# Performance work log

Hardware: AMD Instinct MI355X
Metric: run time of the kernel (lower is better)

## Reference

```python
import jax, jax.numpy as jnp
import numpy as np

EMBED_DIM = 1024
B, S = 4, 2048

def setup_inputs() -> dict:
    key = jax.random.key(0)
    ks = jax.random.split(key, 9)
    D = EMBED_DIM
    scale = 1.0 / np.sqrt(D)
    scale2 = 1.0 / np.sqrt(2 * D)
    return {
        "classical_state": jax.random.normal(ks[0], (B, S, D), jnp.float32),
        "quantum_state": jax.random.normal(ks[1], (B, S, D), jnp.float32),
        "Wc": jax.random.uniform(ks[2], (D, D), jnp.float32, -scale, scale),
        "bc": jax.random.uniform(ks[3], (D,), jnp.float32, -scale, scale),
        "Wq": jax.random.uniform(ks[4], (D, D), jnp.float32, -scale, scale),
        "bq": jax.random.uniform(ks[5], (D,), jnp.float32, -scale, scale),
        "Wg": jax.random.uniform(ks[6], (D, 2 * D), jnp.float32, -scale2, scale2),
        "bg": jax.random.uniform(ks[7], (D,), jnp.float32, -scale2, scale2),
        "temperature": jnp.array(1.0, jnp.float32),
    }

def reference(classical_state, quantum_state, Wc, bc, Wq, bq, Wg, bg, temperature):
    D = classical_state.shape[-1]
    c_proj = jnp.einsum('bsd,ed->bse', classical_state, Wc) + bc  # [B,S,D]
    q_proj = jnp.einsum('bsd,ed->bse', quantum_state, Wq) + bq    # [B,S,D]
    combined = jnp.concatenate([c_proj, q_proj], axis=-1)         # [B,S,2D]
    interface_state = jax.nn.sigmoid(jnp.einsum('bsf,ef->bse', combined, Wg) + bg)
    similarity = jnp.einsum('bsd,btd->bst', c_proj, q_proj) / jnp.sqrt(jnp.asarray(D, c_proj.dtype))
    attention_weights = jax.nn.softmax(similarity / temperature, axis=-1)  # [B,S,S]
    transfer_state = jnp.einsum('bst,btd->bsd', attention_weights, quantum_state)
    return classical_state + interface_state * transfer_state
```

## Files before the change

### kernel.cpp

```cpp
#include <hip/hip_runtime.h>


typedef unsigned short u16;
typedef unsigned char u8;
typedef __bf16 bf16x8 __attribute__((ext_vector_type(8)));
typedef float f32x4 __attribute__((ext_vector_type(4)));

__device__ __forceinline__ u16 f2bf(float f) {
    unsigned int x;
    __builtin_memcpy(&x, &f, 4);
    unsigned int r = x + 0x7FFFu + ((x >> 16) & 1u);
    return (u16)(r >> 16);
}
__device__ __forceinline__ float bf2f(u16 u) {
    unsigned int x = ((unsigned int)u) << 16;
    float f;
    __builtin_memcpy(&f, &x, 4);
    return f;
}
__device__ __forceinline__ u8 f2fp8(float f) {
    int p = __builtin_amdgcn_cvt_pk_fp8_f32(f, f, 0, false);
    return (u8)(p & 0xFF);
}

__device__ __forceinline__ void xcd_tile(int& tx, int& ty) {
    const int gx = gridDim.x;
    const int nwg = gx * gridDim.y;
    const int l = blockIdx.x + gx * blockIdx.y;
    const int per = nwg >> 3;
    const int swz = (l & 7) * per + (l >> 3);
    tx = swz % gx;
    ty = swz / gx;
}

#define GLOBAL_TO_LDS16(gp, lp)                                                           \
    __builtin_amdgcn_global_load_lds((const __attribute__((address_space(1))) void*)(gp), \
                                     (__attribute__((address_space(3))) void*)(lp), 16, 0, 0)

__global__ __launch_bounds__(256, 2) void gemm_proj(
    const u16* __restrict__ A0, long sAz, int lda,
    const u16* __restrict__ Bp, long sBz, int ldb,
    u8* __restrict__ C8, long sCz, int ldc, int K,
    const float* __restrict__ bias, long sBiasZ) {
    __shared__ __align__(16) u16 As[128 * 64];
    __shared__ __align__(16) u16 Bs[128 * 64];

    const int tid  = threadIdx.x;
    const int lane = tid & 63;
    const int wave = tid >> 6;
    const int z    = blockIdx.z;

    const u16* a = A0 + (long)z * sAz;
    const u16* b = Bp + (long)z * sBz;

    int tx, ty;
    xcd_tile(tx, ty);
    const int tileM = ty * 128;
    const int tileN = tx * 128;

    const int wm  = wave >> 1;
    const int wn  = wave & 1;
    const int r16 = lane & 15;
    const int kg  = lane >> 4;

    const int srow = lane >> 3;
    const int sgc  = ((lane & 7) ^ (lane >> 3)) * 8;
    const int swb  = r16 & 7;

    f32x4 acc[4][4] = {};

    for (int k0 = 0; k0 < K; k0 += 64) {
#pragma unroll
        for (int p = 0; p < 4; p++) {
            const int rbase = p * 32 + wave * 8;
            GLOBAL_TO_LDS16(a + (long)(tileM + rbase + srow) * lda + k0 + sgc, &As[rbase * 64]);
            GLOBAL_TO_LDS16(b + (long)(tileN + rbase + srow) * ldb + k0 + sgc, &Bs[rbase * 64]);
        }
        __syncthreads();

        bf16x8 af[2][4], bfr[2][4];
#pragma unroll
        for (int h = 0; h < 2; h++) {
#pragma unroll
            for (int i = 0; i < 4; i++) {
                const int Ra = wm * 64 + i * 16 + r16;
                af[h][i]  = *(const bf16x8*)&As[Ra * 64 + (((h * 4 + kg) ^ swb)) * 8];
                const int Rb = wn * 64 + i * 16 + r16;
                bfr[h][i] = *(const bf16x8*)&Bs[Rb * 64 + (((h * 4 + kg) ^ swb)) * 8];
            }
        }
#pragma unroll
        for (int h = 0; h < 2; h++)
#pragma unroll
            for (int i = 0; i < 4; i++)
#pragma unroll
                for (int j = 0; j < 4; j++)
                    acc[i][j] = __builtin_amdgcn_mfma_f32_16x16x32_bf16(
                        af[h][i], bfr[h][j], acc[i][j], 0, 0, 0);
        __syncthreads();
    }

#pragma unroll
    for (int i = 0; i < 4; i++)
#pragma unroll
        for (int j = 0; j < 4; j++) {
            int col = tileN + wn * 64 + j * 16 + r16;
            float bv = bias[(long)z * sBiasZ + col];
#pragma unroll
            for (int v = 0; v < 4; v++) {
                int row = tileM + wm * 64 + i * 16 + kg * 4 + v;
                C8[(long)z * sCz + (long)row * ldc + col] = f2fp8(acc[i][j][v] + bv);
            }
        }
}

template <int MODE>
__global__ __launch_bounds__(256, 2) void gemm8(
    const u8* __restrict__ A0, const u8* __restrict__ A1, long sAz, int lda, int kSplit,
    const u8* __restrict__ Bp, long sBz, int ldb,
    void* __restrict__ Cp, long cOff, long sCz, int ldc, int K,
    const float* __restrict__ bias, const float* __restrict__ temp,
    const float* __restrict__ cls, const u16* __restrict__ g16,
    float* __restrict__ lsum, long lSz) {
    __shared__ __align__(16) u8 As[128 * 128];
    __shared__ __align__(16) u8 Bs[128 * 128];

    const int tid  = threadIdx.x;
    const int lane = tid & 63;
    const int wave = tid >> 6;
    const int z    = blockIdx.z;

    const u8* a = A0 + (long)z * sAz;
    const u8* b = Bp + (long)z * sBz;

    int tx, ty;
    xcd_tile(tx, ty);
    const int tileM = ty * 128;
    const int tileN = tx * 128;

    const int wm  = wave >> 1;
    const int wn  = wave & 1;
    const int r16 = lane & 15;
    const int kg  = lane >> 4;

    const int srow = lane >> 3;
    const int sgc  = ((lane & 7) ^ (lane >> 3)) * 16;

    f32x4 acc[4][4] = {};

    for (int k0 = 0; k0 < K; k0 += 128) {
        const u8* Ap = a;
        int kA = k0;
        if (MODE == 1 && k0 >= kSplit) { Ap = A1; kA = k0 - kSplit; }

#pragma unroll
        for (int p = 0; p < 4; p++) {
            const int rbase = p * 32 + wave * 8;
            GLOBAL_TO_LDS16(Ap + (long)(tileM + rbase + srow) * lda + kA + sgc, &As[rbase * 128]);
            GLOBAL_TO_LDS16(b + (long)(tileN + rbase + srow) * ldb + k0 + sgc, &Bs[rbase * 128]);
        }
        __syncthreads();

#pragma unroll
        for (int h = 0; h < 4; h++) {
            long af[4], bfr[4];
#pragma unroll
            for (int i = 0; i < 4; i++) {
                const int Ra = wm * 64 + i * 16 + r16;
                af[i]  = *(const long*)&As[Ra * 128 + (((h * 2 + (kg >> 1)) ^ (Ra & 7))) * 16 + (kg & 1) * 8];
                const int Rb = wn * 64 + i * 16 + r16;
                bfr[i] = *(const long*)&Bs[Rb * 128 + (((h * 2 + (kg >> 1)) ^ (Rb & 7))) * 16 + (kg & 1) * 8];
            }
#pragma unroll
            for (int i = 0; i < 4; i++)
#pragma unroll
                for (int j = 0; j < 4; j++)
                    acc[i][j] = __builtin_amdgcn_mfma_f32_16x16x32_fp8_fp8(
                        af[i], bfr[j], acc[i][j], 0, 0, 0);
        }
        __syncthreads();
    }

    float scale = 1.0f;
    if (MODE == 2) scale = 1.0f / (32.0f * temp[0]);

    u16*   C16 = (u16*)Cp;
    u8*    C8  = (u8*)Cp;
    float* C32 = (float*)Cp;

#pragma unroll
    for (int i = 0; i < 4; i++) {
        float rs[4] = {0.f, 0.f, 0.f, 0.f};
#pragma unroll
        for (int j = 0; j < 4; j++) {
            int col = tileN + wn * 64 + j * 16 + r16;
            float bv = (MODE == 1) ? bias[col] : 0.0f;
#pragma unroll
            for (int v = 0; v < 4; v++) {
                int row = tileM + wm * 64 + i * 16 + kg * 4 + v;
                long idx = cOff + (long)z * sCz + (long)row * ldc + col;
                float val = acc[i][j][v];
                if (MODE == 1) {
                    C16[idx] = f2bf(1.0f / (1.0f + __expf(-(val + bv))));
                } else if (MODE == 2) {
                    float e = __expf(val * scale);
                    C8[idx] = f2fp8(e);
                    rs[v] += e;
                } else {
                    float inv = 1.0f / lsum[(long)z * lSz + row];
                    C32[idx] = cls[idx] + bf2f(g16[idx]) * (val * inv);
                }
            }
        }
        if (MODE == 2) {
#pragma unroll
            for (int v = 0; v < 4; v++) {
                float s = rs[v];
#pragma unroll
                for (int off = 1; off < 16; off <<= 1) s += __shfl_xor(s, off, 64);
                if (r16 == 0) {
                    int row = tileM + wm * 64 + i * 16 + kg * 4 + v;
                    atomicAdd(&lsum[(long)z * lSz + row], s);
                }
            }
        }
    }
}

__global__ __launch_bounds__(256) void convert_bf16(const f32x4* __restrict__ s,
                                                    ushort4* __restrict__ d, long n4) {
    long i = (long)blockIdx.x * 256 + threadIdx.x;
    long stride = (long)gridDim.x * 256;
    for (; i < n4; i += stride) {
        f32x4 v = s[i];
        ushort4 o;
        o.x = f2bf(v.x); o.y = f2bf(v.y); o.z = f2bf(v.z); o.w = f2bf(v.w);
        d[i] = o;
    }
}

__global__ __launch_bounds__(256) void convert_fp8(const f32x4* __restrict__ s,
                                                   unsigned int* __restrict__ d, long n4) {
    long i = (long)blockIdx.x * 256 + threadIdx.x;
    long stride = (long)gridDim.x * 256;
    for (; i < n4; i += stride) {
        f32x4 v = s[i];
        int w = __builtin_amdgcn_cvt_pk_fp8_f32(v.x, v.y, 0, false);
        w = __builtin_amdgcn_cvt_pk_fp8_f32(v.z, v.w, w, true);
        d[i] = (unsigned int)w;
    }
}

__global__ __launch_bounds__(256) void zero_f32(float* __restrict__ p, int n) {
    int i = blockIdx.x * 256 + threadIdx.x;
    if (i < n) p[i] = 0.0f;
}

__global__ __launch_bounds__(256) void transpose_fp8(const u16* __restrict__ Q,
                                                     u8* __restrict__ QT, int S, int D) {
    __shared__ u8 tile[64][65];
    int bz = blockIdx.z;
    const u16* q = Q + (long)bz * S * D;
    u8* qt = QT + (long)bz * S * D;
    int t0 = blockIdx.x * 64;
    int d0 = blockIdx.y * 64;
    int c = threadIdx.x & 63;
    int r = threadIdx.x >> 6;
#pragma unroll
    for (int i = 0; i < 16; i++) {
        int tl = r + 4 * i;
        tile[tl][c] = f2fp8(bf2f(q[(long)(t0 + tl) * D + d0 + c]));
    }
    __syncthreads();
#pragma unroll
    for (int i = 0; i < 16; i++) {
        int dl = r + 4 * i;
        qt[(long)(d0 + dl) * S + t0 + c] = tile[c][dl];
    }
}

extern "C" void kernel_launch(void* const* d_in, const int* in_sizes, int n_in,
                              void* d_out, int out_size, void* d_ws, size_t ws_size,
                              hipStream_t stream) {
    (void)in_sizes; (void)n_in; (void)out_size;

    const float* classical = (const float*)d_in[0];
    const float* quantum   = (const float*)d_in[1];
    const float* Wc        = (const float*)d_in[2];
    const float* bc        = (const float*)d_in[3];
    const float* Wq        = (const float*)d_in[4];
    const float* bq        = (const float*)d_in[5];
    const float* Wg        = (const float*)d_in[6];
    const float* bg        = (const float*)d_in[7];
    const float* temp      = (const float*)d_in[8];
    float* out = (float*)d_out;

    const int B = 4, S = 2048, D = 1024;
    const long MD = (long)B * S * D;

    float* l       = (float*)d_ws;
    float* biasCat = l + (long)B * S;
    u16* cls_b = (u16*)(biasCat + 2 * D);
    u16* qnt_b = cls_b + MD;
    u16* Wc_b  = qnt_b + MD;
    u16* Wq_b  = Wc_b + (long)D * D;
    u8*  Wg8   = (u8*)(Wq_b + (long)D * D);
    u8*  cp8   = Wg8 + (long)D * 2 * D;
    u8*  qp8   = cp8 + MD;
    u8*  qT8   = qp8 + MD;
    u8*  P8    = qT8 + MD;
    u16* g     = cls_b;

    const size_t fixed_bytes = (size_t)B * S * 4 + 2 * D * 4 +
        (size_t)(2 * MD + 2 * (long)D * D) * 2 + (size_t)D * 2 * D + 3 * (size_t)MD;
    int CH = 128;
    for (int c = 2048; c >= 128; c >>= 1) {
        if (ws_size >= fixed_bytes + (size_t)B * c * S) { CH = c; break; }
    }

    dim3 blk(256);

    convert_bf16<<<1024, blk, 0, stream>>>((const f32x4*)classical, (ushort4*)cls_b, MD / 4);
    convert_bf16<<<1024, blk, 0, stream>>>((const f32x4*)quantum, (ushort4*)qnt_b, MD / 4);
    convert_bf16<<<256, blk, 0, stream>>>((const f32x4*)Wc, (ushort4*)Wc_b, (long)D * D / 4);
    convert_bf16<<<256, blk, 0, stream>>>((const f32x4*)Wq, (ushort4*)Wq_b, (long)D * D / 4);
    convert_fp8<<<512, blk, 0, stream>>>((const f32x4*)Wg, (unsigned int*)Wg8, (long)D * 2 * D / 4);
    hipMemcpyAsync(biasCat, bc, D * sizeof(float), hipMemcpyDeviceToDevice, stream);
    hipMemcpyAsync(biasCat + D, bq, D * sizeof(float), hipMemcpyDeviceToDevice, stream);
    zero_f32<<<dim3((B * S + 255) / 256), blk, 0, stream>>>(l, B * S);

    gemm_proj<<<dim3(D / 128, (B * S) / 128, 2), blk, 0, stream>>>(
        cls_b, MD, D, Wc_b, (long)D * D, D, cp8, MD, D, D, biasCat, D);

    gemm8<1><<<dim3(D / 128, (B * S) / 128, 1), blk, 0, stream>>>(
        cp8, qp8, 0, D, D, Wg8, 0, 2 * D, g, 0, 0, D, 2 * D,
        bg, nullptr, nullptr, nullptr, nullptr, 0);

    transpose_fp8<<<dim3(S / 64, D / 64, B), blk, 0, stream>>>(qnt_b, qT8, S, D);

    for (int m0 = 0; m0 < S; m0 += CH) {
        gemm8<2><<<dim3(S / 128, CH / 128, B), blk, 0, stream>>>(
            cp8 + (long)m0 * D, nullptr, (long)S * D, D, 1 << 30,
            qp8, (long)S * D, D, P8, 0, (long)CH * S, S, D,
            nullptr, temp, nullptr, nullptr, l + m0, S);
        gemm8<4><<<dim3(D / 128, CH / 128, B), blk, 0, stream>>>(
            P8, nullptr, (long)CH * S, S, 1 << 30, qT8, (long)D * S, S,
            out, (long)m0 * D, (long)S * D, D, S,
            nullptr, nullptr, classical, g, l + m0, S);
    }
}
```

Baseline: 296.5 us.

## Double-buffer FP8 GEMMs with larger 256-row tiles and 512-thread blocks

Replaces the single-buffered 128x128 FP8 GEMM with a templated kernel that uses 256-row tiles (256 or 128 columns), 8 waves per block, and double-buffered LDS. The next K-tile's global-to-LDS loads are interleaved with MFMA phases, and setprio raises wave priority around the MFMA bursts. The intent is to hide global load latency and raise data reuse per tile. In exchange it uses much more LDS per block (up to 128KB), which can limit occupancy. The chunk size minimum also rises to 256 rows.

```diff
diff --git a/kernel.cpp b/kernel.cpp
--- a/kernel.cpp
+++ b/kernel.cpp
@@ -114,16 +114,23 @@
         }
 }
 
-template <int MODE>
-__global__ __launch_bounds__(256, 2) void gemm8(
+template <int MODE, int BN, int WM, int WN>
+__global__ __launch_bounds__(512, 2) void gemm8b(
     const u8* __restrict__ A0, const u8* __restrict__ A1, long sAz, int lda, int kSplit,
     const u8* __restrict__ Bp, long sBz, int ldb,
     void* __restrict__ Cp, long cOff, long sCz, int ldc, int K,
     const float* __restrict__ bias, const float* __restrict__ temp,
     const float* __restrict__ cls, const u16* __restrict__ g16,
     float* __restrict__ lsum, long lSz) {
-    __shared__ __align__(16) u8 As[128 * 128];
-    __shared__ __align__(16) u8 Bs[128 * 128];
+    constexpr int BM  = 256;
+    constexpr int BK  = 128;
+    constexpr int MR  = BM / WM / 16;
+    constexpr int NR  = BN / WN / 16;
+    constexpr int NPH = (MR / 2) * (NR / 2);
+    constexpr int BSTG = BN / 64;
+
+    __shared__ __align__(16) u8 As[2][BM * BK];
+    __shared__ __align__(16) u8 Bs[2][BN * BK];
 
     const int tid  = threadIdx.x;
     const int lane = tid & 63;
@@ -135,50 +142,97 @@
 
     int tx, ty;
     xcd_tile(tx, ty);
-    const int tileM = ty * 128;
-    const int tileN = tx * 128;
-
-    const int wm  = wave >> 1;
-    const int wn  = wave & 1;
+    const int tileM = ty * BM;
+    const int tileN = tx * BN;
+
+    const int wm  = wave / WN;
+    const int wn  = wave % WN;
     const int r16 = lane & 15;
     const int kg  = lane >> 4;
 
     const int srow = lane >> 3;
     const int sgc  = ((lane & 7) ^ (lane >> 3)) * 16;
 
-    f32x4 acc[4][4] = {};
-
-    for (int k0 = 0; k0 < K; k0 += 128) {
+    auto stageA = [&](int buf, int t, int p) {
         const u8* Ap = a;
-        int kA = k0;
-        if (MODE == 1 && k0 >= kSplit) { Ap = A1; kA = k0 - kSplit; }
-
-#pragma unroll
-        for (int p = 0; p < 4; p++) {
-            const int rbase = p * 32 + wave * 8;
-            GLOBAL_TO_LDS16(Ap + (long)(tileM + rbase + srow) * lda + kA + sgc, &As[rbase * 128]);
-            GLOBAL_TO_LDS16(b + (long)(tileN + rbase + srow) * ldb + k0 + sgc, &Bs[rbase * 128]);
-        }
-        __syncthreads();
-
-#pragma unroll
-        for (int h = 0; h < 4; h++) {
-            long af[4], bfr[4];
-#pragma unroll
-            for (int i = 0; i < 4; i++) {
-                const int Ra = wm * 64 + i * 16 + r16;
-                af[i]  = *(const long*)&As[Ra * 128 + (((h * 2 + (kg >> 1)) ^ (Ra & 7))) * 16 + (kg & 1) * 8];
-                const int Rb = wn * 64 + i * 16 + r16;
-                bfr[i] = *(const long*)&Bs[Rb * 128 + (((h * 2 + (kg >> 1)) ^ (Rb & 7))) * 16 + (kg & 1) * 8];
-            }
-#pragma unroll
-            for (int i = 0; i < 4; i++)
-#pragma unroll
-                for (int j = 0; j < 4; j++)
-                    acc[i][j] = __builtin_amdgcn_mfma_f32_16x16x32_fp8_fp8(
-                        af[i], bfr[j], acc[i][j], 0, 0, 0);
-        }
-        __syncthreads();
+        int kA = t * BK;
+        if (MODE == 1 && kA >= kSplit) { Ap = A1; kA -= kSplit; }
+        const int rbase = p * 64 + wave * 8;
+        GLOBAL_TO_LDS16(Ap + (long)(tileM + rbase + srow) * lda + kA + sgc,
+                        &As[buf][rbase * BK]);
+    };
+    auto stageB = [&](int buf, int t, int p) {
+        const int rbase = p * 64 + wave * 8;
+        GLOBAL_TO_LDS16(b + (long)(tileN + rbase + srow) * ldb + t * BK + sgc,
+                        &Bs[buf][rbase * BK]);
+    };
+
+    f32x4 acc[MR][NR] = {};
+
+    const int nt = K / BK;
+#pragma unroll
+    for (int p = 0; p < 4; p++) stageA(0, 0, p);
+#pragma unroll
+    for (int p = 0; p < BSTG; p++) stageB(0, 0, p);
+
+    for (int t = 0; t < nt; t++) {
+        const int cur = t & 1, nxt = cur ^ 1;
+        const bool pf = (t + 1 < nt);
+        asm volatile("s_waitcnt vmcnt(0)" ::: "memory");
+        __builtin_amdgcn_s_barrier();
+        asm volatile("" ::: "memory");
+
+#pragma unroll
+        for (int ph = 0; ph < NPH; ph++) {
+            const int i0 = (ph / (NR / 2)) * 2;
+            const int j0 = (ph % (NR / 2)) * 2;
+
+            long af[2][4], bfv[2][4];
+#pragma unroll
+            for (int ii = 0; ii < 2; ii++) {
+                const int Ra = wm * (BM / WM) + (i0 + ii) * 16 + r16;
+#pragma unroll
+                for (int ks = 0; ks < 4; ks++) {
+                    const int c = 2 * ks + (kg >> 1);
+                    af[ii][ks] = *(const long*)&As[cur][Ra * BK + ((c ^ (Ra & 7)) << 4) + (kg & 1) * 8];
+                }
+            }
+#pragma unroll
+            for (int jj = 0; jj < 2; jj++) {
+                const int Rb = wn * (BN / WN) + (j0 + jj) * 16 + r16;
+#pragma unroll
+                for (int ks = 0; ks < 4; ks++) {
+                    const int c = 2 * ks + (kg >> 1);
+                    bfv[jj][ks] = *(const long*)&Bs[cur][Rb * BK + ((c ^ (Rb & 7)) << 4) + (kg & 1) * 8];
+                }
+            }
+
+            if (pf) {
+                if (BN == 128) {
+                    if (ph == 0) { stageA(nxt, t + 1, 0); stageA(nxt, t + 1, 1); }
+                    if (ph == 1) { stageA(nxt, t + 1, 2); stageA(nxt, t + 1, 3); }
+                    if (ph == 2) { stageB(nxt, t + 1, 0); }
+                    if (ph == 3) { stageB(nxt, t + 1, 1); }
+                } else {
+                    if ((ph & 1) == 0) stageA(nxt, t + 1, ph >> 1);
+                    else               stageB(nxt, t + 1, ph >> 1);
+                }
+            }
+
+            __builtin_amdgcn_s_barrier();
+            __builtin_amdgcn_s_setprio(1);
+#pragma unroll
+            for (int ks = 0; ks < 4; ks++)
+#pragma unroll
+                for (int ii = 0; ii < 2; ii++)
+#pragma unroll
+                    for (int jj = 0; jj < 2; jj++)
+                        acc[i0 + ii][j0 + jj] = __builtin_amdgcn_mfma_f32_16x16x32_fp8_fp8(
+                            af[ii][ks], bfv[jj][ks], acc[i0 + ii][j0 + jj], 0, 0, 0);
+            __builtin_amdgcn_s_setprio(0);
+            __builtin_amdgcn_s_barrier();
+            asm volatile("" ::: "memory");
+        }
     }
 
     float scale = 1.0f;
@@ -189,15 +243,15 @@
     float* C32 = (float*)Cp;
 
 #pragma unroll
-    for (int i = 0; i < 4; i++) {
+    for (int i = 0; i < MR; i++) {
         float rs[4] = {0.f, 0.f, 0.f, 0.f};
 #pragma unroll
-        for (int j = 0; j < 4; j++) {
-            int col = tileN + wn * 64 + j * 16 + r16;
+        for (int j = 0; j < NR; j++) {
+            int col = tileN + wn * (BN / WN) + j * 16 + r16;
             float bv = (MODE == 1) ? bias[col] : 0.0f;
 #pragma unroll
             for (int v = 0; v < 4; v++) {
-                int row = tileM + wm * 64 + i * 16 + kg * 4 + v;
+                int row = tileM + wm * (BM / WM) + i * 16 + kg * 4 + v;
                 long idx = cOff + (long)z * sCz + (long)row * ldc + col;
                 float val = acc[i][j][v];
                 if (MODE == 1) {
@@ -219,7 +273,7 @@
 #pragma unroll
                 for (int off = 1; off < 16; off <<= 1) s += __shfl_xor(s, off, 64);
                 if (r16 == 0) {
-                    int row = tileM + wm * 64 + i * 16 + kg * 4 + v;
+                    int row = tileM + wm * (BM / WM) + i * 16 + kg * 4 + v;
                     atomicAdd(&lsum[(long)z * lSz + row], s);
                 }
             }
@@ -313,12 +367,13 @@
 
     const size_t fixed_bytes = (size_t)B * S * 4 + 2 * D * 4 +
         (size_t)(2 * MD + 2 * (long)D * D) * 2 + (size_t)D * 2 * D + 3 * (size_t)MD;
-    int CH = 128;
-    for (int c = 2048; c >= 128; c >>= 1) {
+    int CH = 256;
+    for (int c = 2048; c >= 256; c >>= 1) {
         if (ws_size >= fixed_bytes + (size_t)B * c * S) { CH = c; break; }
     }
 
     dim3 blk(256);
+    dim3 blk8(512);
 
     convert_bf16<<<1024, blk, 0, stream>>>((const f32x4*)classical, (ushort4*)cls_b, MD / 4);
     convert_bf16<<<1024, blk, 0, stream>>>((const f32x4*)quantum, (ushort4*)qnt_b, MD / 4);
@@ -332,18 +387,18 @@
     gemm_proj<<<dim3(D / 128, (B * S) / 128, 2), blk, 0, stream>>>(
         cls_b, MD, D, Wc_b, (long)D * D, D, cp8, MD, D, D, biasCat, D);
 
-    gemm8<1><<<dim3(D / 128, (B * S) / 128, 1), blk, 0, stream>>>(
+    gemm8b<1, 128, 4, 2><<<dim3(D / 128, (B * S) / 256, 1), blk8, 0, stream>>>(
         cp8, qp8, 0, D, D, Wg8, 0, 2 * D, g, 0, 0, D, 2 * D,
         bg, nullptr, nullptr, nullptr, nullptr, 0);
 
     transpose_fp8<<<dim3(S / 64, D / 64, B), blk, 0, stream>>>(qnt_b, qT8, S, D);
 
     for (int m0 = 0; m0 < S; m0 += CH) {
-        gemm8<2><<<dim3(S / 128, CH / 128, B), blk, 0, stream>>>(
+        gemm8b<2, 256, 2, 4><<<dim3(S / 256, CH / 256, B), blk8, 0, stream>>>(
             cp8 + (long)m0 * D, nullptr, (long)S * D, D, 1 << 30,
             qp8, (long)S * D, D, P8, 0, (long)CH * S, S, D,
             nullptr, temp, nullptr, nullptr, l + m0, S);
-        gemm8<4><<<dim3(D / 128, CH / 128, B), blk, 0, stream>>>(
+        gemm8b<4, 128, 4, 2><<<dim3(D / 128, CH / 256, B), blk8, 0, stream>>>(
             P8, nullptr, (long)CH * S, S, 1 << 30, qT8, (long)D * S, S,
             out, (long)m0 * D, (long)S * D, D, S,
             nullptr, nullptr, classical, g, l + m0, S);
```

Result: slower. 355.9 us (+20.1%).

## Fuse fp32-to-bf16 conversion of activations into projection GEMM loads and merge prep kernels

Applied to the files above, without the earlier changes.

The projection GEMM now reads fp32 classical and quantum inputs directly and converts them to bf16 in registers before writing to LDS. This removes the two large standalone conversion passes and their bf16 intermediate buffers. The weight conversions and the zeroing of the row-sum buffer are merged into a single prep kernel, the bias memcpys are dropped in favour of passing both bias pointers, and the transpose reads fp32 directly. In exchange, the A-operand loads are no longer asynchronous global-to-LDS copies, so the GEMM reads twice as many bytes through registers, with extra conversion ALU work and possible stalls.

```diff
diff --git a/kernel.cpp b/kernel.cpp
--- a/kernel.cpp
+++ b/kernel.cpp
@@ -5,6 +5,7 @@
 typedef unsigned char u8;
 typedef __bf16 bf16x8 __attribute__((ext_vector_type(8)));
 typedef float f32x4 __attribute__((ext_vector_type(4)));
+typedef unsigned short ushort8 __attribute__((ext_vector_type(8)));
 
 __device__ __forceinline__ u16 f2bf(float f) {
     unsigned int x;
@@ -38,10 +39,10 @@
                                      (__attribute__((address_space(3))) void*)(lp), 16, 0, 0)
 
 __global__ __launch_bounds__(256, 2) void gemm_proj(
-    const u16* __restrict__ A0, long sAz, int lda,
+    const float* __restrict__ Ac, const float* __restrict__ Aq, int lda,
     const u16* __restrict__ Bp, long sBz, int ldb,
     u8* __restrict__ C8, long sCz, int ldc, int K,
-    const float* __restrict__ bias, long sBiasZ) {
+    const float* __restrict__ bc, const float* __restrict__ bq) {
     __shared__ __align__(16) u16 As[128 * 64];
     __shared__ __align__(16) u16 Bs[128 * 64];
 
@@ -50,8 +51,9 @@
     const int wave = tid >> 6;
     const int z    = blockIdx.z;
 
-    const u16* a = A0 + (long)z * sAz;
+    const float* a = z ? Aq : Ac;
     const u16* b = Bp + (long)z * sBz;
+    const float* bias = z ? bq : bc;
 
     int tx, ty;
     xcd_tile(tx, ty);
@@ -64,7 +66,7 @@
     const int kg  = lane >> 4;
 
     const int srow = lane >> 3;
-    const int sgc  = ((lane & 7) ^ (lane >> 3)) * 8;
+    const int sgc  = ((lane & 7) ^ srow) * 8;
     const int swb  = r16 & 7;
 
     f32x4 acc[4][4] = {};
@@ -73,8 +75,18 @@
 #pragma unroll
         for (int p = 0; p < 4; p++) {
             const int rbase = p * 32 + wave * 8;
-            GLOBAL_TO_LDS16(a + (long)(tileM + rbase + srow) * lda + k0 + sgc, &As[rbase * 64]);
             GLOBAL_TO_LDS16(b + (long)(tileN + rbase + srow) * ldb + k0 + sgc, &Bs[rbase * 64]);
+        }
+#pragma unroll
+        for (int p = 0; p < 4; p++) {
+            const int rbase = p * 32 + wave * 8;
+            const float* src = a + (long)(tileM + rbase + srow) * lda + k0 + sgc;
+            f32x4 v0 = *(const f32x4*)src;
+            f32x4 v1 = *(const f32x4*)(src + 4);
+            ushort8 w;
+            w[0] = f2bf(v0.x); w[1] = f2bf(v0.y); w[2] = f2bf(v0.z); w[3] = f2bf(v0.w);
+            w[4] = f2bf(v1.x); w[5] = f2bf(v1.y); w[6] = f2bf(v1.z); w[7] = f2bf(v1.w);
+            *(ushort8*)&As[rbase * 64 + lane * 8] = w;
         }
         __syncthreads();
 
@@ -105,7 +117,7 @@
 #pragma unroll
         for (int j = 0; j < 4; j++) {
             int col = tileN + wn * 64 + j * 16 + r16;
-            float bv = bias[(long)z * sBiasZ + col];
+            float bv = bias[col];
 #pragma unroll
             for (int v = 0; v < 4; v++) {
                 int row = tileM + wm * 64 + i * 16 + kg * 4 + v;
@@ -227,40 +239,37 @@
     }
 }
 
-__global__ __launch_bounds__(256) void convert_bf16(const f32x4* __restrict__ s,
-                                                    ushort4* __restrict__ d, long n4) {
+__global__ __launch_bounds__(256) void prep(
+    const f32x4* __restrict__ Wc, const f32x4* __restrict__ Wq, const f32x4* __restrict__ Wg,
+    ushort4* __restrict__ WcB, ushort4* __restrict__ WqB, unsigned int* __restrict__ Wg8,
+    f32x4* __restrict__ l, long nW, long nG, long nL) {
     long i = (long)blockIdx.x * 256 + threadIdx.x;
     long stride = (long)gridDim.x * 256;
-    for (; i < n4; i += stride) {
-        f32x4 v = s[i];
-        ushort4 o;
-        o.x = f2bf(v.x); o.y = f2bf(v.y); o.z = f2bf(v.z); o.w = f2bf(v.w);
-        d[i] = o;
-    }
-}
-
-__global__ __launch_bounds__(256) void convert_fp8(const f32x4* __restrict__ s,
-                                                   unsigned int* __restrict__ d, long n4) {
-    long i = (long)blockIdx.x * 256 + threadIdx.x;
-    long stride = (long)gridDim.x * 256;
-    for (; i < n4; i += stride) {
-        f32x4 v = s[i];
-        int w = __builtin_amdgcn_cvt_pk_fp8_f32(v.x, v.y, 0, false);
-        w = __builtin_amdgcn_cvt_pk_fp8_f32(v.z, v.w, w, true);
-        d[i] = (unsigned int)w;
-    }
-}
-
-__global__ __launch_bounds__(256) void zero_f32(float* __restrict__ p, int n) {
-    int i = blockIdx.x * 256 + threadIdx.x;
-    if (i < n) p[i] = 0.0f;
-}
-
-__global__ __launch_bounds__(256) void transpose_fp8(const u16* __restrict__ Q,
+    long total = 2 * nW + nG + nL;
+    for (; i < total; i += stride) {
+        if (i < 2 * nW) {
+            long j = (i < nW) ? i : i - nW;
+            f32x4 v = (i < nW) ? Wc[j] : Wq[j];
+            ushort4 o;
+            o.x = f2bf(v.x); o.y = f2bf(v.y); o.z = f2bf(v.z); o.w = f2bf(v.w);
+            if (i < nW) WcB[j] = o; else WqB[j] = o;
+        } else if (i < 2 * nW + nG) {
+            long j = i - 2 * nW;
+            f32x4 v = Wg[j];
+            int w = __builtin_amdgcn_cvt_pk_fp8_f32(v.x, v.y, 0, false);
+            w = __builtin_amdgcn_cvt_pk_fp8_f32(v.z, v.w, w, true);
+            Wg8[j] = (unsigned int)w;
+        } else {
+            l[i - 2 * nW - nG] = (f32x4){0.f, 0.f, 0.f, 0.f};
+        }
+    }
+}
+
+__global__ __launch_bounds__(256) void transpose_fp8(const float* __restrict__ Q,
                                                      u8* __restrict__ QT, int S, int D) {
     __shared__ u8 tile[64][65];
     int bz = blockIdx.z;
-    const u16* q = Q + (long)bz * S * D;
+    const float* q = Q + (long)bz * S * D;
     u8* qt = QT + (long)bz * S * D;
     int t0 = blockIdx.x * 64;
     int d0 = blockIdx.y * 64;
@@ -269,7 +278,7 @@
 #pragma unroll
     for (int i = 0; i < 16; i++) {
         int tl = r + 4 * i;
-        tile[tl][c] = f2fp8(bf2f(q[(long)(t0 + tl) * D + d0 + c]));
+        tile[tl][c] = f2fp8(q[(long)(t0 + tl) * D + d0 + c]);
     }
     __syncthreads();
 #pragma unroll
@@ -298,21 +307,18 @@
     const int B = 4, S = 2048, D = 1024;
     const long MD = (long)B * S * D;
 
-    float* l       = (float*)d_ws;
-    float* biasCat = l + (long)B * S;
-    u16* cls_b = (u16*)(biasCat + 2 * D);
-    u16* qnt_b = cls_b + MD;
-    u16* Wc_b  = qnt_b + MD;
-    u16* Wq_b  = Wc_b + (long)D * D;
-    u8*  Wg8   = (u8*)(Wq_b + (long)D * D);
-    u8*  cp8   = Wg8 + (long)D * 2 * D;
-    u8*  qp8   = cp8 + MD;
-    u8*  qT8   = qp8 + MD;
-    u8*  P8    = qT8 + MD;
-    u16* g     = cls_b;
-
-    const size_t fixed_bytes = (size_t)B * S * 4 + 2 * D * 4 +
-        (size_t)(2 * MD + 2 * (long)D * D) * 2 + (size_t)D * 2 * D + 3 * (size_t)MD;
+    float* l    = (float*)d_ws;
+    u16* Wc_b   = (u16*)(l + (long)B * S);
+    u16* Wq_b   = Wc_b + (long)D * D;
+    u8*  Wg8    = (u8*)(Wq_b + (long)D * D);
+    u16* g      = (u16*)(Wg8 + (long)D * 2 * D);
+    u8*  cp8    = (u8*)(g + MD);
+    u8*  qp8    = cp8 + MD;
+    u8*  qT8    = qp8 + MD;
+    u8*  P8     = qT8 + MD;
+
+    const size_t fixed_bytes = (size_t)B * S * 4 + 2 * (size_t)D * D * 2 +
+        (size_t)D * 2 * D + (size_t)MD * 2 + 3 * (size_t)MD;
     int CH = 128;
     for (int c = 2048; c >= 128; c >>= 1) {
         if (ws_size >= fixed_bytes + (size_t)B * c * S) { CH = c; break; }
@@ -320,23 +326,19 @@
 
     dim3 blk(256);
 
-    convert_bf16<<<1024, blk, 0, stream>>>((const f32x4*)classical, (ushort4*)cls_b, MD / 4);
-    convert_bf16<<<1024, blk, 0, stream>>>((const f32x4*)quantum, (ushort4*)qnt_b, MD / 4);
-    convert_bf16<<<256, blk, 0, stream>>>((const f32x4*)Wc, (ushort4*)Wc_b, (long)D * D / 4);
-    convert_bf16<<<256, blk, 0, stream>>>((const f32x4*)Wq, (ushort4*)Wq_b, (long)D * D / 4);
-    convert_fp8<<<512, blk, 0, stream>>>((const f32x4*)Wg, (unsigned int*)Wg8, (long)D * 2 * D / 4);
-    hipMemcpyAsync(biasCat, bc, D * sizeof(float), hipMemcpyDeviceToDevice, stream);
-    hipMemcpyAsync(biasCat + D, bq, D * sizeof(float), hipMemcpyDeviceToDevice, stream);
-    zero_f32<<<dim3((B * S + 255) / 256), blk, 0, stream>>>(l, B * S);
+    prep<<<1024, blk, 0, stream>>>(
+        (const f32x4*)Wc, (const f32x4*)Wq, (const f32x4*)Wg,
+        (ushort4*)Wc_b, (ushort4*)Wq_b, (unsigned int*)Wg8,
+        (f32x4*)l, (long)D * D / 4, (long)D * 2 * D / 4, (long)B * S / 4);
 
     gemm_proj<<<dim3(D / 128, (B * S) / 128, 2), blk, 0, stream>>>(
-        cls_b, MD, D, Wc_b, (long)D * D, D, cp8, MD, D, D, biasCat, D);
+        classical, quantum, D, Wc_b, (long)D * D, D, cp8, MD, D, D, bc, bq);
 
     gemm8<1><<<dim3(D / 128, (B * S) / 128, 1), blk, 0, stream>>>(
         cp8, qp8, 0, D, D, Wg8, 0, 2 * D, g, 0, 0, D, 2 * D,
         bg, nullptr, nullptr, nullptr, nullptr, 0);
 
-    transpose_fp8<<<dim3(S / 64, D / 64, B), blk, 0, stream>>>(qnt_b, qT8, S, D);
+    transpose_fp8<<<dim3(S / 64, D / 64, B), blk, 0, stream>>>(quantum, qT8, S, D);
 
     for (int m0 = 0; m0 < S; m0 += CH) {
         gemm8<2><<<dim3(S / 128, CH / 128, B), blk, 0, stream>>>(
```

Result: no change. 291.3 us (-1.7%).
